# Kernel tuning notes

Hardware: AMD Instinct MI355X
Metric: run time of the kernel (lower is better)

Reference implementation:

```python
import jax, jax.numpy as jnp
import numpy as np
import math

T, B, I, H = 512, 64, 1024, 1024


def setup_inputs() -> dict:
    key = jax.random.key(0)
    ks = jax.random.split(key, 5)
    stdv = 1.0 / math.sqrt(H)
    u = lambda k, shp: jax.random.uniform(k, shp, jnp.float32, -stdv, stdv)
    return {
        "x": jax.random.normal(ks[0], (T, B, I), jnp.float32),
        "c0": jnp.zeros((B, H), jnp.float32),
        "h0": jnp.zeros((B, H), jnp.float32),
        "W_ih": u(ks[1], (I, 4 * H)),
        "W_hh": u(ks[2], (H, 4 * H)),
        "b_ih": u(ks[3], (4 * H,)),
        "b_hh": u(ks[4], (4 * H,)),
    }


def reference(x, c0, h0, W_ih, W_hh, b_ih, b_hh):
    # x: [T, B, I]; standard single-layer LSTM, zero-dropout, seq-major.
    def step(carry, xt):
        h, c = carry
        gates = xt @ W_ih + b_ih + h @ W_hh + b_hh  # [B, 4H]
        i, f, g, o = jnp.split(gates, 4, axis=1)
        i = jax.nn.sigmoid(i)
        f = jax.nn.sigmoid(f)
        g = jnp.tanh(g)
        o = jax.nn.sigmoid(o)
        c_new = f * c + i * g
        h_new = o * jnp.tanh(c_new)
        return (h_new, c_new), h_new

    (h_last, c_last), outputs = jax.lax.scan(step, (h0, c0), x)
    return outputs, h_last, c_last  # outputs: [T, B, H]
```

## Files before the change

kernel.cpp:

```cpp
#include <hip/hip_runtime.h>
#include <stdint.h>
#include <stddef.h>

#define TSEQ 512
#define NB   64
#define DI   1024
#define DHID 1024
#define NG   4096
#define NGRP 4
#define WPG  64
#define NWGS 256
#define FPAD 32

typedef __attribute__((ext_vector_type(8))) short short8;
typedef __attribute__((ext_vector_type(4))) float f32x4;

__device__ __forceinline__ unsigned short f2bf(float f) {
  union { float f; uint32_t u; } v; v.f = f;
  uint32_t u = v.u;
  uint32_t r = u + 0x7fffu + ((u >> 16) & 1u);
  return (unsigned short)(r >> 16);
}
__device__ __forceinline__ float bf2f(unsigned short b) {
  union { uint32_t u; float f; } v; v.u = ((uint32_t)b) << 16;
  return v.f;
}
__device__ __forceinline__ float fsigm(float x) { return 1.0f / (1.0f + __expf(-x)); }
__device__ __forceinline__ float ftanh(float x) { return 1.0f - 2.0f / (__expf(2.0f * x) + 1.0f); }

__device__ __forceinline__ void gll16(const void* g, void* l) {
  __builtin_amdgcn_global_load_lds(
      (const __attribute__((address_space(1))) void*)g,
      (__attribute__((address_space(3))) void*)l, 16, 0, 0);
}

__device__ __forceinline__ void st_dword_llc(void* addr, uint32_t val) {
  asm volatile("global_store_dword %0, %1, off sc0 sc1" :: "v"(addr), "v"(val) : "memory");
}
__device__ __forceinline__ short8 ld_b128_llc(const void* addr) {
  short8 v;
  asm volatile("global_load_dwordx4 %0, %1, off sc0 sc1" : "=v"(v) : "v"(addr) : "memory");
  return v;
}

__global__ void k_convert_x(const float* __restrict__ x, unsigned short* __restrict__ xb, int n4) {
  int idx = blockIdx.x * blockDim.x + threadIdx.x;
  int stride = gridDim.x * blockDim.x;
  const float4* xf = (const float4*)x;
  for (int i = idx; i < n4; i += stride) {
    float4 v = xf[i];
    unsigned short o0 = f2bf(v.x), o1 = f2bf(v.y), o2 = f2bf(v.z), o3 = f2bf(v.w);
    uint2 packed;
    packed.x = (uint32_t)o0 | ((uint32_t)o1 << 16);
    packed.y = (uint32_t)o2 | ((uint32_t)o3 << 16);
    ((uint2*)xb)[i] = packed;
  }
}

__global__ void k_transpose_w(const float* __restrict__ w, unsigned short* __restrict__ wt) {
  __shared__ float tile[32][33];
  int n0 = blockIdx.x * 32;
  int k0 = blockIdx.y * 32;
  int c = threadIdx.x & 31, r0 = threadIdx.x >> 5;
  for (int r = r0; r < 32; r += 8)
    tile[r][c] = w[(size_t)(k0 + r) * NG + n0 + c];
  __syncthreads();
  for (int r = r0; r < 32; r += 8)
    wt[(size_t)(n0 + r) * 1024 + k0 + c] = f2bf(tile[c][r]);
}

__global__ void k_init(const float* __restrict__ h0, const float* __restrict__ b_ih,
                       const float* __restrict__ b_hh, unsigned short* __restrict__ hbuf0,
                       float* __restrict__ bsum, unsigned* __restrict__ arrive) {
  int i = blockIdx.x * 256 + threadIdx.x;
  if (i < NB * DHID) {
    int bg = i >> 10, un = i & 1023;
    int gg = bg >> 4, bb = bg & 15, ww = un >> 4, uu = un & 15;
    hbuf0[((gg * WPG + ww) * 16 + bb) * 16 + uu] = f2bf(h0[i]);
  }
  if (i < NG) bsum[i] = b_ih[i] + b_hh[i];
  if (i < NGRP * WPG * FPAD) arrive[i] = 0u;
}

template <bool PF32>
__global__ __launch_bounds__(256, 2) void k_gemm_pregates(
    const unsigned short* __restrict__ xb,
    const unsigned short* __restrict__ wt,
    void* __restrict__ pg) {
  __shared__ char lds_raw[32768];
  char* As = lds_raw;
  char* Bs = lds_raw + 16384;

  const int wave = threadIdx.x >> 6;
  const int lane = threadIdx.x & 63;
  const int ln = lane & 15, quad = lane >> 4;
  const int m0 = blockIdx.x * 128;
  const int n0 = blockIdx.y * 128;
  const int mw = (wave >> 1) * 64, nw = (wave & 1) * 64;

  f32x4 acc[4][4] = {};

  for (int kc = 0; kc < 16; ++kc) {
    __syncthreads();
#pragma unroll
    for (int i = 0; i < 4; ++i) {
      int s = wave * 256 + i * 64 + lane;
      int row = s >> 3;
      int kg = (s & 7) ^ (row & 7);
      gll16(xb + (size_t)(m0 + row) * 1024 + kc * 64 + kg * 8, As + s * 16);
      gll16(wt + (size_t)(n0 + row) * 1024 + kc * 64 + kg * 8, Bs + s * 16);
    }
    __syncthreads();

    short8 a[2][4], b[2][4];
#pragma unroll
    for (int kt = 0; kt < 2; ++kt) {
      int kg = kt * 4 + quad;
#pragma unroll
      for (int mt = 0; mt < 4; ++mt) {
        int row = mw + mt * 16 + ln;
        a[kt][mt] = *(const short8*)(As + (row * 8 + (kg ^ (row & 7))) * 16);
      }
#pragma unroll
      for (int nt = 0; nt < 4; ++nt) {
        int row = nw + nt * 16 + ln;
        b[kt][nt] = *(const short8*)(Bs + (row * 8 + (kg ^ (row & 7))) * 16);
      }
    }
#pragma unroll
    for (int kt = 0; kt < 2; ++kt)
#pragma unroll
      for (int mt = 0; mt < 4; ++mt)
#pragma unroll
        for (int nt = 0; nt < 4; ++nt)
          acc[mt][nt] = __builtin_amdgcn_mfma_f32_16x16x32_bf16(a[kt][mt], b[kt][nt], acc[mt][nt], 0, 0, 0);
  }

#pragma unroll
  for (int mt = 0; mt < 4; ++mt)
#pragma unroll
    for (int nt = 0; nt < 4; ++nt)
#pragma unroll
      for (int r = 0; r < 4; ++r) {
        int rowg = m0 + mw + mt * 16 + quad * 4 + r;
        int colg = n0 + nw + nt * 16 + ln;
        int t = rowg >> 6, bglob = rowg & 63;
        int gb = bglob >> 4, bl = bglob & 15;
        int gate = colg >> 10, j = colg & 1023;
        int w = j >> 4, u = j & 15;
        size_t idx = (((size_t)t * NGRP + gb) * WPG + w) * 1024 + (size_t)bl * 64 + gate * 16 + u;
        if (PF32)
          ((float*)pg)[idx] = acc[mt][nt][r];
        else
          ((unsigned short*)pg)[idx] = f2bf(acc[mt][nt][r]);
      }
}

template <bool PF32>
__global__ __launch_bounds__(256, 1) void k_lstm(
    const unsigned short* __restrict__ whhT,
    const void* __restrict__ pg,
    const float* __restrict__ c0,
    const float* __restrict__ bsum,
    unsigned short* __restrict__ hbuf,
    float* __restrict__ out,
    unsigned* __restrict__ arrive) {
  const int bid = blockIdx.x;
  const int g = bid >> 6;
  const int w = bid & 63;
  const int tid = threadIdx.x;
  const int wave = tid >> 6, lane = tid & 63;
  const int ln = lane & 15, quad = lane >> 4;

  __shared__ char wlds[4 * 32 * 1024];
  __shared__ float gl2[4][4][16][17];

  unsigned* arr = arrive + g * WPG * FPAD;

  {
    const unsigned short* src = whhT + (size_t)(wave * 1024 + w * 16 + ln) * 1024 + quad * 8;
    char* dst = wlds + wave * 32768;
#pragma unroll
    for (int kt = 0; kt < 32; ++kt)
      gll16(src + kt * 32, dst + kt * 1024);
  }
  __syncthreads();

  const int b = tid >> 4, u = tid & 15;
  const int bg = g * 16 + b;
  const int un = w * 16 + u;
  float cst = c0[(size_t)bg * DHID + un];
  const float bs0 = bsum[un], bs1 = bsum[1024 + un],
              bs2 = bsum[2048 + un], bs3 = bsum[3072 + un];

  const size_t out_hlast = (size_t)TSEQ * NB * DHID;
  const size_t out_clast = out_hlast + (size_t)NB * DHID;

  float p0, p1, p2, p3;
#define LDPG(T)                                                                      \
  {                                                                                  \
    size_t base = (((size_t)(T) * NGRP + g) * WPG + w) * 1024 + (size_t)b * 64 + u;  \
    if (PF32) {                                                                      \
      const float* pp = (const float*)pg;                                            \
      p0 = pp[base]; p1 = pp[base + 16]; p2 = pp[base + 32]; p3 = pp[base + 48];     \
    } else {                                                                         \
      const unsigned short* pp = (const unsigned short*)pg;                          \
      p0 = bf2f(pp[base]); p1 = bf2f(pp[base + 16]);                                 \
      p2 = bf2f(pp[base + 32]); p3 = bf2f(pp[base + 48]);                            \
    }                                                                                \
  }
  LDPG(0);

  for (int t = 0; t < TSEQ; ++t) {
    const unsigned short* hin = hbuf + (size_t)(t & 1) * (NB * DHID);
    unsigned short* hout = hbuf + (size_t)((t + 1) & 1) * (NB * DHID);
    const unsigned short* hg = hin + g * (WPG * 256);

    short8 afr[8];
#pragma unroll
    for (int j = 0; j < 8; ++j) {
      int kt = wave * 8 + j;
      afr[j] = ld_b128_llc(hg + kt * 512 + (quad >> 1) * 256 + ln * 16 + (quad & 1) * 8);
    }
    asm volatile("s_waitcnt vmcnt(0)" ::: "memory");
    __builtin_amdgcn_sched_barrier(0);

    f32x4 acc[4] = {};
#pragma unroll
    for (int gx = 0; gx < 4; ++gx) {
      const char* wbg = wlds + gx * 32768 + (wave * 8) * 1024 + lane * 16;
#pragma unroll
      for (int j = 0; j < 8; ++j) {
        short8 bfr = *(const short8*)(wbg + j * 1024);
        acc[gx] = __builtin_amdgcn_mfma_f32_16x16x32_bf16(afr[j], bfr, acc[gx], 0, 0, 0);
      }
    }
#pragma unroll
    for (int gx = 0; gx < 4; ++gx)
#pragma unroll
      for (int r = 0; r < 4; ++r)
        gl2[wave][gx][quad * 4 + r][ln] = acc[gx][r];
    __syncthreads();

    float gi = ((gl2[0][0][b][u] + gl2[1][0][b][u]) + (gl2[2][0][b][u] + gl2[3][0][b][u])) + p0 + bs0;
    float gf = ((gl2[0][1][b][u] + gl2[1][1][b][u]) + (gl2[2][1][b][u] + gl2[3][1][b][u])) + p1 + bs1;
    float gg = ((gl2[0][2][b][u] + gl2[1][2][b][u]) + (gl2[2][2][b][u] + gl2[3][2][b][u])) + p2 + bs2;
    float go = ((gl2[0][3][b][u] + gl2[1][3][b][u]) + (gl2[2][3][b][u] + gl2[3][3][b][u])) + p3 + bs3;
    float i_ = fsigm(gi), f_ = fsigm(gf), g_ = ftanh(gg), o_ = fsigm(go);
    float cn = f_ * cst + i_ * g_;
    cst = cn;
    float h = o_ * ftanh(cn);
    out[((size_t)t * NB + bg) * DHID + un] = h;

    float hn = __shfl_xor(h, 1);
    if (!(tid & 1)) {
      uint32_t pk = (uint32_t)f2bf(h) | ((uint32_t)f2bf(hn) << 16);
      st_dword_llc((void*)(hout + g * (WPG * 256) + w * 256 + tid), pk);
    }

    if (t == TSEQ - 1) {
      out[out_hlast + (size_t)bg * DHID + un] = h;
      out[out_clast + (size_t)bg * DHID + un] = cn;
    }

    if (t < TSEQ - 1) {
      asm volatile("s_waitcnt vmcnt(0)" ::: "memory");
      __syncthreads();
      if (tid == 0)
        __hip_atomic_store(&arr[w * FPAD], (unsigned)(t + 1), __ATOMIC_RELAXED,
                           __HIP_MEMORY_SCOPE_SYSTEM);
      LDPG(t + 1);
      if (tid < 64) {
        const unsigned tgt = (unsigned)(t + 1);
        while (true) {
          unsigned v = __hip_atomic_load(&arr[tid * FPAD], __ATOMIC_RELAXED,
                                         __HIP_MEMORY_SCOPE_SYSTEM);
          if (__all((int)(v >= tgt))) break;
          __builtin_amdgcn_s_sleep(1);
        }
      }
      __syncthreads();
    }
  }
#undef LDPG
}

static inline size_t align_up(size_t x, size_t a) { return (x + a - 1) & ~(a - 1); }

extern "C" void kernel_launch(void* const* d_in, const int* in_sizes, int n_in,
                              void* d_out, int out_size, void* d_ws, size_t ws_size,
                              hipStream_t stream) {
  const float* x    = (const float*)d_in[0];
  const float* c0   = (const float*)d_in[1];
  const float* h0   = (const float*)d_in[2];
  const float* W_ih = (const float*)d_in[3];
  const float* W_hh = (const float*)d_in[4];
  const float* b_ih = (const float*)d_in[5];
  const float* b_hh = (const float*)d_in[6];
  float* out = (float*)d_out;

  const size_t pg_elems = (size_t)TSEQ * NB * NG;
  const size_t xb_bytes = (size_t)TSEQ * NB * DI * 2;
  const size_t wt_bytes = (size_t)NG * 1024 * 2;
  const size_t hb_bytes = (size_t)2 * NB * DHID * 2;
  const size_t bsum_bytes = (size_t)NG * 4;
  const size_t arr_bytes = (size_t)NGRP * WPG * FPAD * 4;

  auto layout = [&](size_t pg_bytes, size_t* offs) {
    size_t o = 0;
    offs[0] = o; o = align_up(o + pg_bytes, 256);
    offs[1] = o; o = align_up(o + xb_bytes, 256);
    offs[2] = o; o = align_up(o + wt_bytes, 256);
    offs[3] = o; o = align_up(o + wt_bytes, 256);
    offs[4] = o; o = align_up(o + hb_bytes, 256);
    offs[5] = o; o = align_up(o + bsum_bytes, 256);
    offs[6] = o; o = align_up(o + arr_bytes, 256);
    return o;
  };
  size_t offs[7];
  size_t need_f32 = layout(pg_elems * 4, offs);
  bool pf32 = ws_size >= need_f32;
  if (!pf32) layout(pg_elems * 2, offs);

  char* ws = (char*)d_ws;
  void* pg = ws + offs[0];
  unsigned short* xb   = (unsigned short*)(ws + offs[1]);
  unsigned short* wihT = (unsigned short*)(ws + offs[2]);
  unsigned short* whhT = (unsigned short*)(ws + offs[3]);
  unsigned short* hbuf = (unsigned short*)(ws + offs[4]);
  float* bsum = (float*)(ws + offs[5]);
  unsigned* arrive = (unsigned*)(ws + offs[6]);

  k_convert_x<<<2048, 256, 0, stream>>>(x, xb, (int)((size_t)TSEQ * NB * DI / 4));
  k_transpose_w<<<dim3(NG / 32, 1024 / 32), 256, 0, stream>>>(W_ih, wihT);
  k_transpose_w<<<dim3(NG / 32, 1024 / 32), 256, 0, stream>>>(W_hh, whhT);
  k_init<<<(NB * DHID + 255) / 256, 256, 0, stream>>>(h0, b_ih, b_hh, hbuf, bsum, arrive);

  dim3 ggrid(TSEQ * NB / 128, NG / 128);
  if (pf32)
    k_gemm_pregates<true><<<ggrid, 256, 0, stream>>>(xb, wihT, pg);
  else
    k_gemm_pregates<false><<<ggrid, 256, 0, stream>>>(xb, wihT, pg);

  if (pf32)
    k_lstm<true><<<NWGS, 256, 0, stream>>>(whhT, pg, c0, bsum, hbuf, out, arrive);
  else
    k_lstm<false><<<NWGS, 256, 0, stream>>>(whhT, pg, c0, bsum, hbuf, out, arrive);
}
```

Baseline: 2.371 ms.

## Regroup LSTM workgroups into 8 XCC-local groups with register-resident weights

Repartitions the persistent LSTM recurrence from 4 batch groups of 64 workgroups to 8 groups of 32 workgroups. Workgroup ids are mapped so each group can sit on one XCC, and a startup vote checks that every member of the group runs on the matching XCC. When the vote passes, h exchange and flag polling use sc0-only (non-LLC) loads and stores, with a periodic full-scope poll as fallback. W_hh slices move from LDS into VGPRs (64 short8 per thread), and the pregate layout changes to match. The aim is to cut cross-die synchronisation latency per timestep, at the cost of heavy register pressure and a dependence on hardware scheduling placement.

```diff
diff --git a/kernel.cpp b/kernel.cpp
--- a/kernel.cpp
+++ b/kernel.cpp
@@ -7,8 +7,8 @@
 #define DI   1024
 #define DHID 1024
 #define NG   4096
-#define NGRP 4
-#define WPG  64
+#define NGRP 8
+#define WPG  32
 #define NWGS 256
 #define FPAD 32
 
@@ -34,12 +34,20 @@
       (__attribute__((address_space(3))) void*)l, 16, 0, 0);
 }
 
-__device__ __forceinline__ void st_dword_llc(void* addr, uint32_t val) {
-  asm volatile("global_store_dword %0, %1, off sc0 sc1" :: "v"(addr), "v"(val) : "memory");
-}
-__device__ __forceinline__ short8 ld_b128_llc(const void* addr) {
+template <bool LOCAL> __device__ __forceinline__ void st_u32(void* a, uint32_t v) {
+  if (LOCAL) asm volatile("global_store_dword %0, %1, off sc0" :: "v"(a), "v"(v) : "memory");
+  else       asm volatile("global_store_dword %0, %1, off sc0 sc1" :: "v"(a), "v"(v) : "memory");
+}
+template <bool LOCAL> __device__ __forceinline__ uint32_t ld_u32(const void* a) {
+  uint32_t v;
+  if (LOCAL) asm volatile("global_load_dword %0, %1, off sc0" : "=v"(v) : "v"(a) : "memory");
+  else       asm volatile("global_load_dword %0, %1, off sc0 sc1" : "=v"(v) : "v"(a) : "memory");
+  return v;
+}
+template <bool LOCAL> __device__ __forceinline__ short8 ld_b128(const void* a) {
   short8 v;
-  asm volatile("global_load_dwordx4 %0, %1, off sc0 sc1" : "=v"(v) : "v"(addr) : "memory");
+  if (LOCAL) asm volatile("global_load_dwordx4 %0, %1, off sc0" : "=v"(v) : "v"(a) : "memory");
+  else       asm volatile("global_load_dwordx4 %0, %1, off sc0 sc1" : "=v"(v) : "v"(a) : "memory");
   return v;
 }
 
@@ -75,11 +83,11 @@
   int i = blockIdx.x * 256 + threadIdx.x;
   if (i < NB * DHID) {
     int bg = i >> 10, un = i & 1023;
-    int gg = bg >> 4, bb = bg & 15, ww = un >> 4, uu = un & 15;
-    hbuf0[((gg * WPG + ww) * 16 + bb) * 16 + uu] = f2bf(h0[i]);
+    int gg = bg >> 3, bb = bg & 7, ww = un >> 5, uu = un & 31;
+    hbuf0[(((size_t)gg * WPG + ww) * 8 + bb) * 32 + uu] = f2bf(h0[i]);
   }
   if (i < NG) bsum[i] = b_ih[i] + b_hh[i];
-  if (i < NGRP * WPG * FPAD) arrive[i] = 0u;
+  if (i < NGRP * WPG * FPAD * 2) arrive[i] = 0u;
 }
 
 template <bool PF32>
@@ -145,15 +153,147 @@
         int rowg = m0 + mw + mt * 16 + quad * 4 + r;
         int colg = n0 + nw + nt * 16 + ln;
         int t = rowg >> 6, bglob = rowg & 63;
-        int gb = bglob >> 4, bl = bglob & 15;
+        int gb = bglob >> 3, bl = bglob & 7;
         int gate = colg >> 10, j = colg & 1023;
-        int w = j >> 4, u = j & 15;
-        size_t idx = (((size_t)t * NGRP + gb) * WPG + w) * 1024 + (size_t)bl * 64 + gate * 16 + u;
+        int w = j >> 5, uu = j & 31;
+        size_t idx = (((size_t)t * NGRP + gb) * WPG + w) * 1024 + (size_t)gate * 256 + bl * 32 + uu;
         if (PF32)
           ((float*)pg)[idx] = acc[mt][nt][r];
         else
           ((unsigned short*)pg)[idx] = f2bf(acc[mt][nt][r]);
       }
+}
+
+template <bool LOCAL, bool PF32>
+__device__ __forceinline__ void lstm_loop(
+    const unsigned short* __restrict__ whhT, const void* __restrict__ pg,
+    const float* __restrict__ c0, const float* __restrict__ bsum,
+    unsigned short* __restrict__ hbuf, float* __restrict__ out,
+    unsigned* __restrict__ flags, float (*gl2)[8][8][17], int g, int w) {
+  const int tid = threadIdx.x;
+  const int wave = tid >> 6, lane = tid & 63;
+  const int ln = lane & 15, quad = lane >> 4;
+
+  short8 wreg[8][8];
+#pragma unroll
+  for (int cb = 0; cb < 8; ++cb) {
+    const unsigned short* wcol = whhT +
+        (size_t)((cb >> 1) * 1024 + w * 32 + (cb & 1) * 16 + ln) * 1024 +
+        wave * 256 + quad * 8;
+#pragma unroll
+    for (int kt = 0; kt < 8; ++kt)
+      wreg[cb][kt] = *(const short8*)(wcol + kt * 32);
+  }
+#pragma unroll
+  for (int cb = 0; cb < 8; ++cb)
+#pragma unroll
+    for (int kt = 0; kt < 8; ++kt)
+      asm volatile("" : "+v"(wreg[cb][kt]));
+
+  const int b = tid >> 5, u = tid & 31;
+  const int bg = g * 8 + b;
+  const int un = w * 32 + u;
+  float cst = c0[(size_t)bg * DHID + un];
+  const float bs0 = bsum[un], bs1 = bsum[1024 + un],
+              bs2 = bsum[2048 + un], bs3 = bsum[3072 + un];
+
+  const size_t out_hlast = (size_t)TSEQ * NB * DHID;
+  const size_t out_clast = out_hlast + (size_t)NB * DHID;
+
+  float p0, p1, p2, p3;
+#define LDPG(T)                                                                      \
+  {                                                                                  \
+    size_t base = (((size_t)(T) * NGRP + g) * WPG + w) * 1024 + (size_t)b * 32 + u;  \
+    if (PF32) {                                                                      \
+      const float* pp = (const float*)pg;                                            \
+      p0 = pp[base]; p1 = pp[base + 256]; p2 = pp[base + 512]; p3 = pp[base + 768];  \
+    } else {                                                                         \
+      const unsigned short* pp = (const unsigned short*)pg;                          \
+      p0 = bf2f(pp[base]); p1 = bf2f(pp[base + 256]);                                \
+      p2 = bf2f(pp[base + 512]); p3 = bf2f(pp[base + 768]);                          \
+    }                                                                                \
+  }
+  LDPG(0);
+
+  const int hoff_a = (ln & 7) * 32 + quad * 8;
+
+  for (int t = 0; t < TSEQ; ++t) {
+    const unsigned short* hg = hbuf + (size_t)(t & 1) * (NB * DHID) + (size_t)g * (WPG * 256);
+    unsigned short* hog = hbuf + (size_t)((t + 1) & 1) * (NB * DHID) +
+                          (size_t)g * (WPG * 256) + w * 256;
+
+    short8 afr[8];
+#pragma unroll
+    for (int j = 0; j < 8; ++j)
+      afr[j] = ld_b128<LOCAL>(hg + (wave * 8 + j) * 256 + hoff_a);
+    asm volatile("s_waitcnt vmcnt(0)" ::: "memory");
+    __builtin_amdgcn_sched_barrier(0);
+
+    f32x4 acc[8] = {};
+#pragma unroll
+    for (int j = 0; j < 8; ++j)
+#pragma unroll
+      for (int cb = 0; cb < 8; ++cb)
+        acc[cb] = __builtin_amdgcn_mfma_f32_16x16x32_bf16(afr[j], wreg[cb][j], acc[cb], 0, 0, 0);
+
+    if (quad < 2) {
+#pragma unroll
+      for (int cb = 0; cb < 8; ++cb)
+#pragma unroll
+        for (int r = 0; r < 4; ++r)
+          gl2[wave][cb][quad * 4 + r][ln] = acc[cb][r];
+    }
+    __syncthreads();
+
+    const int cbl = u >> 4, lnl = u & 15;
+    float gi = ((gl2[0][0 + cbl][b][lnl] + gl2[1][0 + cbl][b][lnl]) +
+                (gl2[2][0 + cbl][b][lnl] + gl2[3][0 + cbl][b][lnl])) + p0 + bs0;
+    float gf = ((gl2[0][2 + cbl][b][lnl] + gl2[1][2 + cbl][b][lnl]) +
+                (gl2[2][2 + cbl][b][lnl] + gl2[3][2 + cbl][b][lnl])) + p1 + bs1;
+    float gg = ((gl2[0][4 + cbl][b][lnl] + gl2[1][4 + cbl][b][lnl]) +
+                (gl2[2][4 + cbl][b][lnl] + gl2[3][4 + cbl][b][lnl])) + p2 + bs2;
+    float go = ((gl2[0][6 + cbl][b][lnl] + gl2[1][6 + cbl][b][lnl]) +
+                (gl2[2][6 + cbl][b][lnl] + gl2[3][6 + cbl][b][lnl])) + p3 + bs3;
+    float i_ = fsigm(gi), f_ = fsigm(gf), g_ = ftanh(gg), o_ = fsigm(go);
+    float cn = f_ * cst + i_ * g_;
+    cst = cn;
+    float h = o_ * ftanh(cn);
+    out[((size_t)t * NB + bg) * DHID + un] = h;
+
+    float hn = __shfl_xor(h, 1);
+    if (!(u & 1)) {
+      uint32_t pk = (uint32_t)f2bf(h) | ((uint32_t)f2bf(hn) << 16);
+      st_u32<LOCAL>((void*)(hog + b * 32 + u), pk);
+    }
+
+    if (t == TSEQ - 1) {
+      out[out_hlast + (size_t)bg * DHID + un] = h;
+      out[out_clast + (size_t)bg * DHID + un] = cn;
+    }
+
+    if (t < TSEQ - 1) {
+      asm volatile("s_waitcnt vmcnt(0)" ::: "memory");
+      __syncthreads();
+      if (tid == 0) st_u32<false>((void*)(flags + w * FPAD), (uint32_t)(t + 1));
+      LDPG(t + 1);
+      if (tid < 64) {
+        const unsigned tgt = (unsigned)(t + 1);
+        int it = 0;
+        while (true) {
+          unsigned v;
+          if (LOCAL && ((++it) & 7))
+            v = ld_u32<true>((const void*)(flags + (tid & 31) * FPAD));
+          else
+            v = ld_u32<false>((const void*)(flags + (tid & 31) * FPAD));
+          asm volatile("s_waitcnt vmcnt(0)" ::: "memory");
+          if (__all((int)(v >= tgt))) break;
+          __builtin_amdgcn_s_sleep(1);
+        }
+      }
+      __syncthreads();
+    }
+  }
+#undef LDPG
 }
 
 template <bool PF32>
@@ -166,123 +306,37 @@
     float* __restrict__ out,
     unsigned* __restrict__ arrive) {
   const int bid = blockIdx.x;
-  const int g = bid >> 6;
-  const int w = bid & 63;
+  const int g = bid & 7;
+  const int w = bid >> 3;
   const int tid = threadIdx.x;
-  const int wave = tid >> 6, lane = tid & 63;
-  const int ln = lane & 15, quad = lane >> 4;
-
-  __shared__ char wlds[4 * 32 * 1024];
-  __shared__ float gl2[4][4][16][17];
-
-  unsigned* arr = arrive + g * WPG * FPAD;
-
-  {
-    const unsigned short* src = whhT + (size_t)(wave * 1024 + w * 16 + ln) * 1024 + quad * 8;
-    char* dst = wlds + wave * 32768;
-#pragma unroll
-    for (int kt = 0; kt < 32; ++kt)
-      gll16(src + kt * 32, dst + kt * 1024);
+
+  __shared__ float gl2s[4][8][8][17];
+  __shared__ int smode;
+
+  unsigned* flags = arrive + (size_t)g * WPG * FPAD;
+  unsigned* votes = arrive + (size_t)NGRP * WPG * FPAD + (size_t)g * WPG * FPAD;
+
+  int xcc;
+  asm volatile("s_getreg_b32 %0, hwreg(HW_REG_XCC_ID)" : "=s"(xcc));
+  unsigned myvote = (xcc == g) ? 1u : 2u;
+  if (tid == 0) st_u32<false>((void*)(votes + w * FPAD), myvote);
+  if (tid < 64) {
+    int loc = 0;
+    while (true) {
+      unsigned v = ld_u32<false>((const void*)(votes + (tid & 31) * FPAD));
+      asm volatile("s_waitcnt vmcnt(0)" ::: "memory");
+      if (__all((int)(v != 0u))) { loc = __all((int)(v == 1u)); break; }
+      __builtin_amdgcn_s_sleep(2);
+    }
+    if (tid == 0) smode = loc;
   }
   __syncthreads();
-
-  const int b = tid >> 4, u = tid & 15;
-  const int bg = g * 16 + b;
-  const int un = w * 16 + u;
-  float cst = c0[(size_t)bg * DHID + un];
-  const float bs0 = bsum[un], bs1 = bsum[1024 + un],
-              bs2 = bsum[2048 + un], bs3 = bsum[3072 + un];
-
-  const size_t out_hlast = (size_t)TSEQ * NB * DHID;
-  const size_t out_clast = out_hlast + (size_t)NB * DHID;
-
-  float p0, p1, p2, p3;
-#define LDPG(T)                                                                      \
-  {                                                                                  \
-    size_t base = (((size_t)(T) * NGRP + g) * WPG + w) * 1024 + (size_t)b * 64 + u;  \
-    if (PF32) {                                                                      \
-      const float* pp = (const float*)pg;                                            \
-      p0 = pp[base]; p1 = pp[base + 16]; p2 = pp[base + 32]; p3 = pp[base + 48];     \
-    } else {                                                                         \
-      const unsigned short* pp = (const unsigned short*)pg;                          \
-      p0 = bf2f(pp[base]); p1 = bf2f(pp[base + 16]);                                 \
-      p2 = bf2f(pp[base + 32]); p3 = bf2f(pp[base + 48]);                            \
-    }                                                                                \
-  }
-  LDPG(0);
-
-  for (int t = 0; t < TSEQ; ++t) {
-    const unsigned short* hin = hbuf + (size_t)(t & 1) * (NB * DHID);
-    unsigned short* hout = hbuf + (size_t)((t + 1) & 1) * (NB * DHID);
-    const unsigned short* hg = hin + g * (WPG * 256);
-
-    short8 afr[8];
-#pragma unroll
-    for (int j = 0; j < 8; ++j) {
-      int kt = wave * 8 + j;
-      afr[j] = ld_b128_llc(hg + kt * 512 + (quad >> 1) * 256 + ln * 16 + (quad & 1) * 8);
-    }
-    asm volatile("s_waitcnt vmcnt(0)" ::: "memory");
-    __builtin_amdgcn_sched_barrier(0);
-
-    f32x4 acc[4] = {};
-#pragma unroll
-    for (int gx = 0; gx < 4; ++gx) {
-      const char* wbg = wlds + gx * 32768 + (wave * 8) * 1024 + lane * 16;
-#pragma unroll
-      for (int j = 0; j < 8; ++j) {
-        short8 bfr = *(const short8*)(wbg + j * 1024);
-        acc[gx] = __builtin_amdgcn_mfma_f32_16x16x32_bf16(afr[j], bfr, acc[gx], 0, 0, 0);
-      }
-    }
-#pragma unroll
-    for (int gx = 0; gx < 4; ++gx)
-#pragma unroll
-      for (int r = 0; r < 4; ++r)
-        gl2[wave][gx][quad * 4 + r][ln] = acc[gx][r];
-    __syncthreads();
-
-    float gi = ((gl2[0][0][b][u] + gl2[1][0][b][u]) + (gl2[2][0][b][u] + gl2[3][0][b][u])) + p0 + bs0;
-    float gf = ((gl2[0][1][b][u] + gl2[1][1][b][u]) + (gl2[2][1][b][u] + gl2[3][1][b][u])) + p1 + bs1;
-    float gg = ((gl2[0][2][b][u] + gl2[1][2][b][u]) + (gl2[2][2][b][u] + gl2[3][2][b][u])) + p2 + bs2;
-    float go = ((gl2[0][3][b][u] + gl2[1][3][b][u]) + (gl2[2][3][b][u] + gl2[3][3][b][u])) + p3 + bs3;
-    float i_ = fsigm(gi), f_ = fsigm(gf), g_ = ftanh(gg), o_ = fsigm(go);
-    float cn = f_ * cst + i_ * g_;
-    cst = cn;
-    float h = o_ * ftanh(cn);
-    out[((size_t)t * NB + bg) * DHID + un] = h;
-
-    float hn = __shfl_xor(h, 1);
-    if (!(tid & 1)) {
-      uint32_t pk = (uint32_t)f2bf(h) | ((uint32_t)f2bf(hn) << 16);
-      st_dword_llc((void*)(hout + g * (WPG * 256) + w * 256 + tid), pk);
-    }
-
-    if (t == TSEQ - 1) {
-      out[out_hlast + (size_t)bg * DHID + un] = h;
-      out[out_clast + (size_t)bg * DHID + un] = cn;
-    }
-
-    if (t < TSEQ - 1) {
-      asm volatile("s_waitcnt vmcnt(0)" ::: "memory");
-      __syncthreads();
-      if (tid == 0)
-        __hip_atomic_store(&arr[w * FPAD], (unsigned)(t + 1), __ATOMIC_RELAXED,
-                           __HIP_MEMORY_SCOPE_SYSTEM);
-      LDPG(t + 1);
-      if (tid < 64) {
-        const unsigned tgt = (unsigned)(t + 1);
-        while (true) {
-          unsigned v = __hip_atomic_load(&arr[tid * FPAD], __ATOMIC_RELAXED,
-                                         __HIP_MEMORY_SCOPE_SYSTEM);
-          if (__all((int)(v >= tgt))) break;
-          __builtin_amdgcn_s_sleep(1);
-        }
-      }
-      __syncthreads();
-    }
-  }
-#undef LDPG
+  const int local = smode;
+
+  if (local)
+    lstm_loop<true, PF32>(whhT, pg, c0, bsum, hbuf, out, flags, gl2s, g, w);
+  else
+    lstm_loop<false, PF32>(whhT, pg, c0, bsum, hbuf, out, flags, gl2s, g, w);
 }
 
 static inline size_t align_up(size_t x, size_t a) { return (x + a - 1) & ~(a - 1); }
@@ -304,7 +358,7 @@
   const size_t wt_bytes = (size_t)NG * 1024 * 2;
   const size_t hb_bytes = (size_t)2 * NB * DHID * 2;
   const size_t bsum_bytes = (size_t)NG * 4;
-  const size_t arr_bytes = (size_t)NGRP * WPG * FPAD * 4;
+  const size_t arr_bytes = (size_t)NGRP * WPG * FPAD * 4 * 2;
 
   auto layout = [&](size_t pg_bytes, size_t* offs) {
     size_t o = 0;
```

Measured after the change: 2.477 ms. 1.04x slower.
